# Kernel tuning notes

Hardware: AMD Instinct MI355X
Metric: run time of the kernel (lower is better)

The kernel has to match this reference:

```python
import jax, jax.numpy as jnp
import numpy as np

B, K, N, E, T = 4096, 64, 100000, 128, 3


def setup_inputs() -> dict:
    key = jax.random.key(0)
    ks = jax.random.split(key, 16)
    f = lambda i, shape: jax.random.normal(ks[i], shape, dtype=jnp.float32) * 0.05
    return dict(
        nodes=jax.random.randint(ks[0], (B,), 0, N),
        neigh_idx=jax.random.randint(ks[1], (T, B, K), 0, N),
        node_emb=f(2, (N, E)),
        node_prof=f(3, (N, E)),
        neigh_emb=f(4, (T, N, E)),
        neigh_prof=f(5, (T, N, E)),
        W_f=f(6, (2 * E, E)), b_f=jnp.zeros((E,), jnp.float32),
        Wa1=f(7, (2 * E, E)), ba1=jnp.zeros((E,), jnp.float32),
        Wa2=f(8, (E, E)), ba2=jnp.zeros((E,), jnp.float32),
        Wa3=f(9, (E, 1)), ba3=jnp.zeros((1,), jnp.float32),
        W1=f(10, (E, E)), b1=jnp.zeros((E,), jnp.float32),
        W2=f(11, (E, E)), b2=jnp.zeros((E,), jnp.float32),
        Wc=f(12, (2 * E, E)), bc=jnp.zeros((E,), jnp.float32),
        Wt=f(13, (T * E, T)),
    )


def reference(nodes, neigh_idx, node_emb, node_prof, neigh_emb, neigh_prof,
              W_f, b_f, Wa1, ba1, Wa2, ba2, Wa3, ba3,
              W1, b1, W2, b2, Wc, bc, Wt):
    # fusion(emb, profile) = relu(Linear(concat(emb, profile)))
    fuse = lambda e, p: jax.nn.relu(jnp.concatenate([e, p], -1) @ W_f + b_f)

    nodes_fusion = fuse(node_emb[nodes], node_prof[nodes])            # [B,E]

    per_type = []
    for t in range(T):                                                 # small fixed loop over types
        idx = neigh_idx[t]                                             # [B,K]
        nf = fuse(neigh_emb[t][idx], neigh_prof[t][idx])               # [B,K,E]
        # attention MLP over (neighbor, node) pairs -> softmax over K neighbors
        x = jnp.concatenate(
            [nf, jnp.broadcast_to(nodes_fusion[:, None, :], nf.shape)], -1)  # [B,K,2E]
        h = jax.nn.relu(x @ Wa1 + ba1)
        h = jax.nn.relu(h @ Wa2 + ba2)
        att = jax.nn.softmax((h @ Wa3 + ba3).squeeze(-1), axis=1)      # [B,K]
        agg = jnp.einsum('bke,bk->be', nf, att)                        # weighted neighbor sum
        per_type.append(jax.nn.relu(agg @ W1 + b1))                    # linear_1 + relu

    type_agg = jnp.concatenate(per_type, axis=1)                       # [B,T*E]
    att_t = jax.nn.softmax(type_agg @ Wt, axis=1)                      # [B,T]
    final = jnp.einsum('bte,bt->be', type_agg.reshape(B, T, E), att_t)
    final = jax.nn.relu(final @ W2 + b2)                               # linear_2 + relu
    out = jax.nn.relu(jnp.concatenate([nodes_fusion, final], 1) @ Wc + bc)
    return out, att_t[:, :, None]
```

## Files before the change

### kernel.cpp

```cpp
#include <hip/hip_runtime.h>
#include <hip/hip_bf16.h>

#define B_ 4096
#define K_ 64
#define N_ 100000
#define E_ 128
#define T_ 3

typedef __bf16 bf16x8 __attribute__((ext_vector_type(8)));
typedef float  f32x4  __attribute__((ext_vector_type(4)));

static __device__ __forceinline__ bf16x8 cvt8r(f32x4 u, f32x4 v) {
    bf16x8 o;
    o[0] = (__bf16)u[0]; o[1] = (__bf16)u[1]; o[2] = (__bf16)u[2]; o[3] = (__bf16)u[3];
    o[4] = (__bf16)v[0]; o[5] = (__bf16)v[1]; o[6] = (__bf16)v[2]; o[7] = (__bf16)v[3];
    return o;
}

typedef const __attribute__((address_space(1))) void GAS;
typedef __attribute__((address_space(3))) void LAS;
static __device__ __forceinline__ void gload16(const void* g, void* l) {
    __builtin_amdgcn_global_load_lds((GAS*)g, (LAS*)l, 16, 0, 0);
}

#define MFMA16(a, b, c) __builtin_amdgcn_mfma_f32_16x16x32_bf16((a), (b), (c), 0, 0, 0)

__global__ __launch_bounds__(256)
void k_prep(const float* __restrict__ W_f, const float* __restrict__ Wa1,
            const float* __restrict__ Wa2, const float* __restrict__ W1,
            __bf16* __restrict__ WtF, __bf16* __restrict__ Wa1t,
            __bf16* __restrict__ Wa2t, __bf16* __restrict__ W1t) {
    const int n = blockIdx.x;
    const int k = threadIdx.x;
    if (blockIdx.y == 0) {
        WtF[n * 256 + k] = (__bf16)W_f[k * 128 + n];
    } else if (blockIdx.y == 1) {
        if (k < 128) Wa1t[n * 128 + k] = (__bf16)Wa1[k * 128 + n];
    } else if (blockIdx.y == 2) {
        if (k < 128) Wa2t[n * 128 + k] = (__bf16)Wa2[k * 128 + n];
    } else {
        if (k < 128) W1t[n * 128 + k] = (__bf16)W1[k * 128 + n];
    }
}

__global__ __launch_bounds__(128)
void k_node_fusion(const int* __restrict__ nodes,
                   const float* __restrict__ node_emb,
                   const float* __restrict__ node_prof,
                   const float* __restrict__ W_f, const float* __restrict__ b_f,
                   __bf16* __restrict__ nodes_fusion) {
    __shared__ float x[256];
    const int b = blockIdx.x;
    const int e = threadIdx.x;
    const int nd = nodes[b];
    x[e]       = node_emb[(size_t)nd * E_ + e];
    x[128 + e] = node_prof[(size_t)nd * E_ + e];
    __syncthreads();
    float acc = b_f[e];
#pragma unroll 8
    for (int i = 0; i < 256; ++i) acc = fmaf(x[i], W_f[i * E_ + e], acc);
    nodes_fusion[(size_t)b * E_ + e] = (__bf16)fmaxf(acc, 0.f);
}

__global__ __launch_bounds__(128)
void k_node_pre(const __bf16* __restrict__ nodes_fusion,
                const float* __restrict__ Wa1, const float* __restrict__ ba1,
                float* __restrict__ node_pre) {
    __shared__ float x[128];
    const int b = blockIdx.x;
    const int c = threadIdx.x;
    x[c] = (float)nodes_fusion[(size_t)b * E_ + c];
    __syncthreads();
    float acc = ba1[c];
#pragma unroll 8
    for (int i = 0; i < 128; ++i) acc = fmaf(x[i], Wa1[(128 + i) * E_ + c], acc);
    node_pre[(size_t)b * E_ + c] = acc;
}

#define NF_GRID 1024
#define NF_TPT (N_ / 16)
#define NF_NJOB (NF_TPT * T_)

__global__ __launch_bounds__(256, 4)
void k_nf(const float* __restrict__ neigh_emb,
          const float* __restrict__ neigh_prof,
          const __bf16* __restrict__ WtF, const float* __restrict__ b_f,
          __bf16* __restrict__ NFt) {
    __shared__ __align__(16) float  Xf[2][16 * 256];
    __shared__ __align__(16) __bf16 NFl[16 * 128];

    const int tid  = threadIdx.x;
    const int wid  = tid >> 6, lane = tid & 63;
    const int lr   = lane & 15, lk = lane >> 4;

    bf16x8 wf[16];
#pragma unroll
    for (int ks = 0; ks < 8; ++ks)
#pragma unroll
        for (int n = 0; n < 2; ++n)
            wf[ks * 2 + n] = *(const bf16x8*)&WtF[
                (size_t)(wid * 32 + n * 16 + lr) * 256 + ks * 32 + lk * 8];
    const float bb0 = b_f[wid * 32 + lr];
    const float bb1 = b_f[wid * 32 + 16 + lr];

    auto stage = [&](int j, int buf) {
        const int t    = j / NF_TPT;
        const int base = (j - t * NF_TPT) * 16;
        const float* embT  = neigh_emb  + (size_t)t * N_ * E_;
        const float* profT = neigh_prof + (size_t)t * N_ * E_;
#pragma unroll
        for (int i = 0; i < 4; ++i) {
            const int r  = wid * 4 + i;
            const int id = base + r;
            const int g  = lane ^ (r & 15);
            const float* src = (g < 32)
                ? embT  + (size_t)id * E_ + g * 4
                : profT + (size_t)id * E_ + (g - 32) * 4;
            gload16(src, (char*)&Xf[buf][0] + r * 1024);
        }
    };

    int job = blockIdx.x;
    stage(job, 0);
    int cur = 0;
    bool first = true;

    for (; job < NF_NJOB; job += NF_GRID) {
        const int tc    = job / NF_TPT;
        const int basec = (job - tc * NF_TPT) * 16;

        if (first) { asm volatile("s_waitcnt vmcnt(0)" ::: "memory"); first = false; }
        else       { asm volatile("s_waitcnt vmcnt(1)" ::: "memory"); }
        __builtin_amdgcn_s_barrier();
        __builtin_amdgcn_sched_barrier(0);

        const int nxt = job + NF_GRID;
        if (nxt < NF_NJOB) stage(nxt, cur ^ 1);

        const float* X = &Xf[cur][0];

        {
            f32x4 acc1[2] = {};
#pragma unroll
            for (int ks = 0; ks < 8; ++ks) {
                const int g0 = ks * 8 + lk * 2;
                const f32x4 u0 = *(const f32x4*)&X[lr * 256 + ((g0 ^ lr) << 2)];
                const f32x4 v0 = *(const f32x4*)&X[lr * 256 + (((g0 + 1) ^ lr) << 2)];
                const bf16x8 a0 = cvt8r(u0, v0);
                acc1[0] = MFMA16(a0, wf[ks * 2 + 0], acc1[0]);
                acc1[1] = MFMA16(a0, wf[ks * 2 + 1], acc1[1]);
            }
#pragma unroll
            for (int n = 0; n < 2; ++n) {
                const int c = wid * 32 + n * 16 + lr;
                const float bb = n ? bb1 : bb0;
                const int q = c >> 3, eo = c & 7;
#pragma unroll
                for (int j = 0; j < 4; ++j) {
                    const int rN = lk * 4 + j;
                    NFl[rN * 128 + ((q ^ rN) << 3) + eo] =
                        (__bf16)fmaxf(acc1[n][j] + bb, 0.f);
                }
            }
        }
        asm volatile("s_waitcnt lgkmcnt(0)" ::: "memory");
        __builtin_amdgcn_s_barrier();
        __builtin_amdgcn_sched_barrier(0);

        {
            const int rr = tid >> 4, qq = tid & 15;
            const int p = qq ^ (rr & 15);
            __bf16* outp = NFt + ((size_t)tc * N_ + basec + rr) * E_ + qq * 8;
            *(bf16x8*)outp = *(const bf16x8*)&NFl[rr * 128 + (p << 3)];
        }
        cur ^= 1;
    }
}

#define ATT_GRID 512
#define ATT_NJOB (B_ * T_)
#define ATT_NITER (ATT_NJOB / ATT_GRID)

__global__ __launch_bounds__(256, 2)
void k_att(const int* __restrict__ neigh_idx,
           const __bf16* __restrict__ NFt,
           const __bf16* __restrict__ Wa1t,
           const __bf16* __restrict__ Wa2t,
           const float* __restrict__ ba2,
           const float* __restrict__ Wa3, const float* __restrict__ ba3,
           const float* __restrict__ node_pre,
           __bf16* __restrict__ aggB) {
    __shared__ __align__(16) __bf16 Nb[2][64 * 128];
    __shared__ __align__(16) __bf16 H1l[64 * 128];
    __shared__ float scp[4 * 64];
    __shared__ float red4[4 * 128];

    const int tid = threadIdx.x;
    const int wid = tid >> 6, lane = tid & 63;
    const int lr = lane & 15, lk = lane >> 4;

    bf16x8 wa1r[8], wa2r[8];
#pragma unroll
    for (int ks = 0; ks < 4; ++ks)
#pragma unroll
        for (int n = 0; n < 2; ++n) {
            wa1r[ks * 2 + n] = *(const bf16x8*)&Wa1t[
                (size_t)(wid * 32 + n * 16 + lr) * 128 + ks * 32 + lk * 8];
            wa2r[ks * 2 + n] = *(const bf16x8*)&Wa2t[
                (size_t)(wid * 32 + n * 16 + lr) * 128 + ks * 32 + lk * 8];
        }
    float ba2r[2], wa3r[2];
#pragma unroll
    for (int n = 0; n < 2; ++n) {
        ba2r[n] = ba2[wid * 32 + n * 16 + lr];
        wa3r[n] = Wa3[wid * 32 + n * 16 + lr];
    }
    const float ba3v = ba3[0];

    auto stage = [&](int j, int buf, int idv) {
        const int t = j / B_;
        const __bf16* tab = NFt + (size_t)t * N_ * E_;
#pragma unroll
        for (int i = 0; i < 4; ++i) {
            const int rowblock = wid * 16 + i * 4;
            const int rsub = i * 4 + (lane >> 4);
            const int q = (lane & 15) ^ rsub;
            const int id = __shfl(idv, rsub);
            gload16(tab + (size_t)id * E_ + q * 8,
                    (char*)&Nb[buf][0] + rowblock * 256);
        }
    };

    int job = blockIdx.x;
    {
        const int idv0 = neigh_idx[(size_t)job * K_ + wid * 16 + (lane & 15)];
        stage(job, 0, idv0);
    }
    float npn0 = node_pre[(size_t)(job % B_) * E_ + wid * 32 + lr];
    float npn1 = node_pre[(size_t)(job % B_) * E_ + wid * 32 + 16 + lr];
    int jn = job + ATT_GRID; if (jn >= ATT_NJOB) jn = ATT_NJOB - 1;
    int idnext = neigh_idx[(size_t)jn * K_ + wid * 16 + (lane & 15)];
    int cur = 0;

    for (int it = 0; it < ATT_NITER; ++it, job += ATT_GRID) {
        asm volatile("s_waitcnt vmcnt(0)" ::: "memory");
        __builtin_amdgcn_s_barrier();
        __builtin_amdgcn_sched_barrier(0);

        const float np0 = npn0, np1 = npn1;

        if (it + 1 < ATT_NITER) {
            stage(job + ATT_GRID, cur ^ 1, idnext);
            int j2 = job + 2 * ATT_GRID; if (j2 >= ATT_NJOB) j2 = ATT_NJOB - 1;
            idnext = neigh_idx[(size_t)j2 * K_ + wid * 16 + (lane & 15)];
            const int bn = (job + ATT_GRID) % B_;
            npn0 = node_pre[(size_t)bn * E_ + wid * 32 + lr];
            npn1 = node_pre[(size_t)bn * E_ + wid * 32 + 16 + lr];
        }

        const __bf16* NbC = &Nb[cur][0];

        {
            f32x4 acc2[4][2] = {};
#pragma unroll
            for (int ks = 0; ks < 4; ++ks) {
                const int q = ks * 4 + lk;
                bf16x8 a[4];
#pragma unroll
                for (int mi = 0; mi < 4; ++mi)
                    a[mi] = *(const bf16x8*)&NbC[(mi * 16 + lr) * 128 + ((q ^ lr) << 3)];
#pragma unroll
                for (int n = 0; n < 2; ++n)
#pragma unroll
                    for (int mi = 0; mi < 4; ++mi)
                        acc2[mi][n] = MFMA16(a[mi], wa1r[ks * 2 + n], acc2[mi][n]);
            }
#pragma unroll
            for (int n = 0; n < 2; ++n) {
                const int col = wid * 32 + n * 16 + lr;
                const float pp = n ? np1 : np0;
                const int q = col >> 3, eo = col & 7;
#pragma unroll
                for (int mi = 0; mi < 4; ++mi)
#pragma unroll
                    for (int j = 0; j < 4; ++j) {
                        const int row = mi * 16 + lk * 4 + j;
                        H1l[row * 128 + ((q ^ (row & 15)) << 3) + eo] =
                            (__bf16)fmaxf(acc2[mi][n][j] + pp, 0.f);
                    }
            }
        }
        asm volatile("s_waitcnt lgkmcnt(0)" ::: "memory");
        __builtin_amdgcn_s_barrier();
        __builtin_amdgcn_sched_barrier(0);

        {
            f32x4 acc3[4][2] = {};
#pragma unroll
            for (int ks = 0; ks < 4; ++ks) {
                const int q = ks * 4 + lk;
                bf16x8 a[4];
#pragma unroll
                for (int mi = 0; mi < 4; ++mi)
                    a[mi] = *(const bf16x8*)&H1l[(mi * 16 + lr) * 128 + ((q ^ lr) << 3)];
#pragma unroll
                for (int n = 0; n < 2; ++n)
#pragma unroll
                    for (int mi = 0; mi < 4; ++mi)
                        acc3[mi][n] = MFMA16(a[mi], wa2r[ks * 2 + n], acc3[mi][n]);
            }
#pragma unroll
            for (int mi = 0; mi < 4; ++mi)
#pragma unroll
                for (int j = 0; j < 4; ++j) {
                    float v = fmaxf(acc3[mi][0][j] + ba2r[0], 0.f) * wa3r[0]
                            + fmaxf(acc3[mi][1][j] + ba2r[1], 0.f) * wa3r[1];
                    v += __shfl_xor(v, 1);
                    v += __shfl_xor(v, 2);
                    v += __shfl_xor(v, 4);
                    v += __shfl_xor(v, 8);
                    if (lr == 0)
                        scp[wid * 64 + mi * 16 + lk * 4 + j] = v;
                }
        }
        asm volatile("s_waitcnt lgkmcnt(0)" ::: "memory");
        __builtin_amdgcn_s_barrier();
        __builtin_amdgcn_sched_barrier(0);

        float att;
        {
            const float v = scp[lane] + scp[64 + lane] + scp[128 + lane]
                          + scp[192 + lane] + ba3v;
            float m = v;
#pragma unroll
            for (int o = 32; o > 0; o >>= 1) m = fmaxf(m, __shfl_xor(m, o));
            const float pe = __expf(v - m);
            float s = pe;
#pragma unroll
            for (int o = 32; o > 0; o >>= 1) s += __shfl_xor(s, o);
            att = pe / s;
        }

        {
            float p0 = 0.f, p1 = 0.f;
            const int q0 = lane >> 3, eo = lane & 7;
            const int q1 = (lane + 64) >> 3;
#pragma unroll
            for (int i = 0; i < 16; ++i) {
                const int row = wid * 16 + i;
                const float av = __shfl(att, row);
                p0 = fmaf(av, (float)NbC[row * 128 + ((q0 ^ (row & 15)) << 3) + eo], p0);
                p1 = fmaf(av, (float)NbC[row * 128 + ((q1 ^ (row & 15)) << 3) + eo], p1);
            }
            red4[wid * 128 + lane] = p0;
            red4[wid * 128 + 64 + lane] = p1;
        }
        asm volatile("s_waitcnt lgkmcnt(0)" ::: "memory");
        __builtin_amdgcn_s_barrier();
        __builtin_amdgcn_sched_barrier(0);

        if (tid < 128) {
            const float s = red4[tid] + red4[128 + tid] + red4[256 + tid]
                          + red4[384 + tid];
            const int bcur = job % B_, tcur = job / B_;
            aggB[((size_t)bcur * T_ + tcur) * E_ + tid] = (__bf16)s;
        }
        cur ^= 1;
    }
}

__global__ __launch_bounds__(256)
void k_w1(const __bf16* __restrict__ aggB, const __bf16* __restrict__ W1t,
          const float* __restrict__ b1, __bf16* __restrict__ type_agg) {
    const int tid  = threadIdx.x;
    const int wid  = tid >> 6;
    const int lane = tid & 63;
    const int lr   = lane & 15;
    const int lk   = lane >> 4;
    const int rbase = blockIdx.x * 64 + wid * 16;

    f32x4 acc[8] = {};
#pragma unroll
    for (int ks = 0; ks < 4; ++ks) {
        const bf16x8 a = *(const bf16x8*)&aggB[(size_t)(rbase + lr) * 128 + ks * 32 + lk * 8];
        const __bf16* wb = W1t + (size_t)lr * 128 + ks * 32 + lk * 8;
#pragma unroll
        for (int n = 0; n < 8; ++n) {
            const bf16x8 w = *(const bf16x8*)(wb + (size_t)n * 16 * 128);
            acc[n] = MFMA16(a, w, acc[n]);
        }
    }
#pragma unroll
    for (int n = 0; n < 8; ++n) {
        const int col = n * 16 + lr;
        const float bb = b1[col];
#pragma unroll
        for (int j = 0; j < 4; ++j) {
            const int row = rbase + lk * 4 + j;
            type_agg[(size_t)row * 128 + col] = (__bf16)fmaxf(acc[n][j] + bb, 0.f);
        }
    }
}

__global__ __launch_bounds__(128)
void k_final(const __bf16* __restrict__ type_agg,
             const __bf16* __restrict__ nodes_fusion,
             const float* __restrict__ Wt,
             const float* __restrict__ W2, const float* __restrict__ b2,
             const float* __restrict__ Wc, const float* __restrict__ bc,
             float* __restrict__ out, float* __restrict__ att_out) {
    __shared__ float ta[384];
    __shared__ float nfu[128];
    __shared__ float fin[128];
    __shared__ float hb[128];
    __shared__ float att[3];
    __shared__ float red[3][128];

    const int b = blockIdx.x;
    const int e = threadIdx.x;

    const float v0 = (float)type_agg[(size_t)b * 384 + e];
    const float v1 = (float)type_agg[(size_t)b * 384 + 128 + e];
    const float v2 = (float)type_agg[(size_t)b * 384 + 256 + e];
    ta[e] = v0; ta[128 + e] = v1; ta[256 + e] = v2;
    nfu[e] = (float)nodes_fusion[(size_t)b * E_ + e];

    float p0, p1, p2;
    {
        const float* w0 = Wt + (size_t)e * 3;
        const float* w1 = Wt + (size_t)(128 + e) * 3;
        const float* w2 = Wt + (size_t)(256 + e) * 3;
        p0 = v0 * w0[0] + v1 * w1[0] + v2 * w2[0];
        p1 = v0 * w0[1] + v1 * w1[1] + v2 * w2[1];
        p2 = v0 * w0[2] + v1 * w1[2] + v2 * w2[2];
    }
    red[0][e] = p0; red[1][e] = p1; red[2][e] = p2;
    __syncthreads();

    if (e < 3) {
        float s = 0.f;
        for (int i = 0; i < 128; ++i) s += red[e][i];
        red[e][0] = s;
    }
    __syncthreads();
    if (e == 0) {
        const float s0 = red[0][0], s1 = red[1][0], s2 = red[2][0];
        const float m  = fmaxf(s0, fmaxf(s1, s2));
        const float e0 = __expf(s0 - m), e1 = __expf(s1 - m), e2 = __expf(s2 - m);
        const float inv = 1.f / (e0 + e1 + e2);
        att[0] = e0 * inv; att[1] = e1 * inv; att[2] = e2 * inv;
    }
    __syncthreads();

    fin[e] = att[0] * ta[e] + att[1] * ta[128 + e] + att[2] * ta[256 + e];
    __syncthreads();

    float acc = b2[e];
#pragma unroll 8
    for (int i = 0; i < 128; ++i) acc = fmaf(fin[i], W2[i * E_ + e], acc);
    hb[e] = fmaxf(acc, 0.f);
    __syncthreads();

    float acc2 = bc[e];
#pragma unroll 8
    for (int i = 0; i < 128; ++i) acc2 = fmaf(nfu[i], Wc[i * E_ + e], acc2);
#pragma unroll 8
    for (int i = 0; i < 128; ++i) acc2 = fmaf(hb[i], Wc[(128 + i) * E_ + e], acc2);
    out[(size_t)b * E_ + e] = fmaxf(acc2, 0.f);

    if (e < 3) att_out[(size_t)b * 3 + e] = att[e];
}

extern "C" void kernel_launch(void* const* d_in, const int* in_sizes, int n_in,
                              void* d_out, int out_size, void* d_ws, size_t ws_size,
                              hipStream_t stream) {
    const int*   nodes      = (const int*)d_in[0];
    const int*   neigh_idx  = (const int*)d_in[1];
    const float* node_emb   = (const float*)d_in[2];
    const float* node_prof  = (const float*)d_in[3];
    const float* neigh_emb  = (const float*)d_in[4];
    const float* neigh_prof = (const float*)d_in[5];
    const float* W_f = (const float*)d_in[6];  const float* b_f = (const float*)d_in[7];
    const float* Wa1 = (const float*)d_in[8];  const float* ba1 = (const float*)d_in[9];
    const float* Wa2 = (const float*)d_in[10]; const float* ba2 = (const float*)d_in[11];
    const float* Wa3 = (const float*)d_in[12]; const float* ba3 = (const float*)d_in[13];
    const float* W1  = (const float*)d_in[14]; const float* b1  = (const float*)d_in[15];
    const float* W2  = (const float*)d_in[16]; const float* b2  = (const float*)d_in[17];
    const float* Wc  = (const float*)d_in[18]; const float* bc  = (const float*)d_in[19];
    const float* Wt  = (const float*)d_in[20];

    float* out     = (float*)d_out;
    float* att_out = out + (size_t)B_ * E_;

    char* ws = (char*)d_ws;
    __bf16* nodes_fusion = (__bf16*)(ws);
    float*  node_pre     = (float*)(ws + (1u << 20));
    __bf16* type_agg     = (__bf16*)(ws + (3u << 20));
    __bf16* aggB         = (__bf16*)(ws + (6u << 20));
    __bf16* WtF          = (__bf16*)(ws + (9u << 20));
    __bf16* Wa1t         = (__bf16*)(ws + (9u << 20) + 65536);
    __bf16* Wa2t         = (__bf16*)(ws + (9u << 20) + 98304);
    __bf16* W1t          = (__bf16*)(ws + (9u << 20) + 131072);
    __bf16* NFt          = (__bf16*)(ws + (16u << 20));

    k_prep<<<dim3(128, 4), 256, 0, stream>>>(W_f, Wa1, Wa2, W1, WtF, Wa1t, Wa2t, W1t);
    k_node_fusion<<<B_, 128, 0, stream>>>(nodes, node_emb, node_prof, W_f, b_f,
                                          nodes_fusion);
    k_node_pre<<<B_, 128, 0, stream>>>(nodes_fusion, Wa1, ba1, node_pre);
    k_nf<<<NF_GRID, 256, 0, stream>>>(neigh_emb, neigh_prof, WtF, b_f, NFt);
    k_att<<<ATT_GRID, 256, 0, stream>>>(neigh_idx, NFt, Wa1t, Wa2t, ba2,
                                        Wa3, ba3, node_pre, aggB);
    k_w1<<<(B_ * T_) / 64, 256, 0, stream>>>(aggB, W1t, b1, type_agg);
    k_final<<<B_, 128, 0, stream>>>(type_agg, nodes_fusion, Wt, W2, b2, Wc, bc,
                                    out, att_out);
}
```

Measured before the change: 300.4 us.

## Triple-buffer neighbor gathers in attention kernel with contiguous per-block job ranges

The attention kernel now gives each block a contiguous range of 24 jobs instead of striding across the grid. It preloads that range's neighbor indices and bf16 node_pre rows into LDS, and it triple-buffers the gathered neighbor tiles so loads run two jobs ahead, using partial vmcnt waits. node_pre is stored in bf16 and the reduction scratch reuses the H1 buffer to save LDS. The aim is to hide gather latency better and cut per-iteration global loads of indices and node_pre, at the cost of more LDS (which may reduce occupancy) and a small precision loss in node_pre.

```diff
diff --git a/kernel.cpp b/kernel.cpp
--- a/kernel.cpp
+++ b/kernel.cpp
@@ -65,7 +65,7 @@
 __global__ __launch_bounds__(128)
 void k_node_pre(const __bf16* __restrict__ nodes_fusion,
                 const float* __restrict__ Wa1, const float* __restrict__ ba1,
-                float* __restrict__ node_pre) {
+                __bf16* __restrict__ node_pre) {
     __shared__ float x[128];
     const int b = blockIdx.x;
     const int c = threadIdx.x;
@@ -74,7 +74,7 @@
     float acc = ba1[c];
 #pragma unroll 8
     for (int i = 0; i < 128; ++i) acc = fmaf(x[i], Wa1[(128 + i) * E_ + c], acc);
-    node_pre[(size_t)b * E_ + c] = acc;
+    node_pre[(size_t)b * E_ + c] = (__bf16)acc;
 }
 
 #define NF_GRID 1024
@@ -178,8 +178,7 @@
 }
 
 #define ATT_GRID 512
-#define ATT_NJOB (B_ * T_)
-#define ATT_NITER (ATT_NJOB / ATT_GRID)
+#define ATT_JPB 24
 
 __global__ __launch_bounds__(256, 2)
 void k_att(const int* __restrict__ neigh_idx,
@@ -188,16 +187,20 @@
            const __bf16* __restrict__ Wa2t,
            const float* __restrict__ ba2,
            const float* __restrict__ Wa3, const float* __restrict__ ba3,
-           const float* __restrict__ node_pre,
+           const __bf16* __restrict__ node_pre,
            __bf16* __restrict__ aggB) {
-    __shared__ __align__(16) __bf16 Nb[2][64 * 128];
+    __shared__ __align__(16) __bf16 Nb[3][64 * 128];
     __shared__ __align__(16) __bf16 H1l[64 * 128];
-    __shared__ float scp[4 * 64];
-    __shared__ float red4[4 * 128];
+    __shared__ int    idxL[ATT_JPB * 64];
+    __shared__ __bf16 npreL[ATT_JPB * 128];
+    __shared__ float  scp[4 * 64];
+
+    float* red4 = (float*)H1l;
 
     const int tid = threadIdx.x;
     const int wid = tid >> 6, lane = tid & 63;
     const int lr = lane & 15, lk = lane >> 4;
+    const int job0 = blockIdx.x * ATT_JPB;
 
     bf16x8 wa1r[8], wa2r[8];
 #pragma unroll
@@ -217,48 +220,44 @@
     }
     const float ba3v = ba3[0];
 
-    auto stage = [&](int j, int buf, int idv) {
-        const int t = j / B_;
+#pragma unroll
+    for (int i = tid; i < ATT_JPB * 64; i += 256)
+        idxL[i] = neigh_idx[(size_t)job0 * K_ + i];
+#pragma unroll
+    for (int i = tid; i < ATT_JPB * 128; i += 256) {
+        const int jj = i >> 7, c = i & 127;
+        const int b = (job0 + jj) % B_;
+        npreL[i] = node_pre[(size_t)b * E_ + c];
+    }
+    __syncthreads();
+
+    auto stage = [&](int jj, int buf) {
+        const int t = (job0 + jj) / B_;
         const __bf16* tab = NFt + (size_t)t * N_ * E_;
 #pragma unroll
         for (int i = 0; i < 4; ++i) {
             const int rowblock = wid * 16 + i * 4;
             const int rsub = i * 4 + (lane >> 4);
             const int q = (lane & 15) ^ rsub;
-            const int id = __shfl(idv, rsub);
+            const int id = idxL[jj * 64 + wid * 16 + rsub];
             gload16(tab + (size_t)id * E_ + q * 8,
                     (char*)&Nb[buf][0] + rowblock * 256);
         }
     };
 
-    int job = blockIdx.x;
-    {
-        const int idv0 = neigh_idx[(size_t)job * K_ + wid * 16 + (lane & 15)];
-        stage(job, 0, idv0);
-    }
-    float npn0 = node_pre[(size_t)(job % B_) * E_ + wid * 32 + lr];
-    float npn1 = node_pre[(size_t)(job % B_) * E_ + wid * 32 + 16 + lr];
-    int jn = job + ATT_GRID; if (jn >= ATT_NJOB) jn = ATT_NJOB - 1;
-    int idnext = neigh_idx[(size_t)jn * K_ + wid * 16 + (lane & 15)];
-    int cur = 0;
-
-    for (int it = 0; it < ATT_NITER; ++it, job += ATT_GRID) {
-        asm volatile("s_waitcnt vmcnt(0)" ::: "memory");
+    stage(0, 0);
+    stage(1, 1);
+
+    for (int it = 0; it < ATT_JPB; ++it) {
+        if (it == 0)                 { asm volatile("s_waitcnt vmcnt(4)" ::: "memory"); }
+        else if (it >= ATT_JPB - 2)  { asm volatile("s_waitcnt vmcnt(0)" ::: "memory"); }
+        else                         { asm volatile("s_waitcnt vmcnt(5)" ::: "memory"); }
         __builtin_amdgcn_s_barrier();
         __builtin_amdgcn_sched_barrier(0);
 
-        const float np0 = npn0, np1 = npn1;
-
-        if (it + 1 < ATT_NITER) {
-            stage(job + ATT_GRID, cur ^ 1, idnext);
-            int j2 = job + 2 * ATT_GRID; if (j2 >= ATT_NJOB) j2 = ATT_NJOB - 1;
-            idnext = neigh_idx[(size_t)j2 * K_ + wid * 16 + (lane & 15)];
-            const int bn = (job + ATT_GRID) % B_;
-            npn0 = node_pre[(size_t)bn * E_ + wid * 32 + lr];
-            npn1 = node_pre[(size_t)bn * E_ + wid * 32 + 16 + lr];
-        }
-
-        const __bf16* NbC = &Nb[cur][0];
+        if (it + 2 < ATT_JPB) stage(it + 2, (it + 2) % 3);
+
+        const __bf16* NbC = &Nb[it % 3][0];
 
         {
             f32x4 acc2[4][2] = {};
@@ -278,7 +277,7 @@
 #pragma unroll
             for (int n = 0; n < 2; ++n) {
                 const int col = wid * 32 + n * 16 + lr;
-                const float pp = n ? np1 : np0;
+                const float pp = (float)npreL[it * 128 + col];
                 const int q = col >> 3, eo = col & 7;
 #pragma unroll
                 for (int mi = 0; mi < 4; ++mi)
@@ -359,13 +358,13 @@
         __builtin_amdgcn_s_barrier();
         __builtin_amdgcn_sched_barrier(0);
 
-        if (tid < 128) {
-            const float s = red4[tid] + red4[128 + tid] + red4[256 + tid]
-                          + red4[384 + tid];
+        if (lane < 32) {
+            const int e = wid * 32 + lane;
+            const float s = red4[e] + red4[128 + e] + red4[256 + e] + red4[384 + e];
+            const int job = job0 + it;
             const int bcur = job % B_, tcur = job / B_;
-            aggB[((size_t)bcur * T_ + tcur) * E_ + tid] = (__bf16)s;
-        }
-        cur ^= 1;
+            aggB[((size_t)bcur * T_ + tcur) * E_ + e] = (__bf16)s;
+        }
     }
 }
 
@@ -494,7 +493,7 @@
 
     char* ws = (char*)d_ws;
     __bf16* nodes_fusion = (__bf16*)(ws);
-    float*  node_pre     = (float*)(ws + (1u << 20));
+    __bf16* node_pre     = (__bf16*)(ws + (1u << 20));
     __bf16* type_agg     = (__bf16*)(ws + (3u << 20));
     __bf16* aggB         = (__bf16*)(ws + (6u << 20));
     __bf16* WtF          = (__bf16*)(ws + (9u << 20));
```

Result: no change. 301.5 us (+0.4%).
